# Performance work log

Hardware: AMD Instinct MI355X
Metric: run time of the kernel (lower is better)

The kernel has to match this reference:

```python
import jax, jax.numpy as jnp
import numpy as np

B = 65536
HID = 128
OUT = 10


def setup_inputs() -> dict:
    key = jax.random.key(0)
    ks = jax.random.split(key, 6)
    x = jax.random.normal(ks[0], (B, 784), dtype=jnp.float32)
    conv_w = jax.random.normal(ks[1], (3, 3), dtype=jnp.float32)
    # torch Linear(676,128): weight [128,676], bias [128]
    w1 = jax.random.normal(ks[2], (HID, 26 * 26), dtype=jnp.float32) * (1.0 / np.sqrt(26 * 26))
    b1 = jax.random.normal(ks[3], (HID,), dtype=jnp.float32) * 0.01
    w2 = jax.random.normal(ks[4], (OUT, HID), dtype=jnp.float32) * (1.0 / np.sqrt(HID))
    b2 = jax.random.normal(ks[5], (OUT,), dtype=jnp.float32) * 0.01
    return {"x": x, "conv_w": conv_w, "w1": w1, "b1": b1, "w2": w2, "b2": b2}


def reference(x, conv_w, w1, b1, w2, b2):
    b = x.shape[0]
    img = x.reshape(b, 1, 28, 28)                      # NCHW, single channel
    kern = conv_w.reshape(1, 1, 3, 3)                  # OIHW
    # valid 3x3 cross-correlation (matches the elementwise-multiply-and-sum loop)
    conv = jax.lax.conv_general_dilated(
        img, kern, window_strides=(1, 1), padding="VALID",
        dimension_numbers=("NCHW", "OIHW", "NCHW"))   # [B,1,26,26]
    feat = conv.reshape(b, 26 * 26)
    h = jax.nn.relu(feat @ w1.T + b1)                  # [B,128]
    return h @ w2.T + b2                               # [B,10]
```

## Files before the change

kernel.cpp:

```cpp
#include <hip/hip_runtime.h>
#include <hip/hip_bf16.h>

#define BATCH  65536
#define KREAL  784
#define BK     64
#define NCHUNK 13
#define HID    128
#define NOUT   10
#define BM     128
#define NTHR   512

using f32x4  = __attribute__((ext_vector_type(4))) float;
using short8 = __attribute__((ext_vector_type(8))) short;
using short4v= __attribute__((ext_vector_type(4))) short;
using f4     = __attribute__((ext_vector_type(4))) float;

__device__ inline short f2b(float f) {
    union { __hip_bfloat16 h; short s; } u;
    u.h = __float2bfloat16(f);
    return u.s;
}

#define GLDS16(gp, lp) \
    __builtin_amdgcn_global_load_lds((const __attribute__((address_space(1))) void*)(gp), \
                                     (__attribute__((address_space(3))) void*)(lp), 16, 0, 0)

#define NWB (NCHUNK*HID*BK)
#define NW2 (4*4*16*8)

__global__ void prep_kernel(const float* __restrict__ conv_w,
                            const float* __restrict__ w1,
                            const float* __restrict__ w2,
                            unsigned short* __restrict__ weff_sw,
                            unsigned short* __restrict__ w2f)
{
    int idx = blockIdx.x * 256 + threadIdx.x;
    if (idx < NWB) {
        int ic  = idx >> 13;
        int rem = idx & 8191;
        int r   = rem >> 6;
        int cc  = rem & 63;
        int g   = (cc >> 3) ^ (r & 7);
        int k   = ic * BK + g * 8 + (cc & 7);
        float acc = 0.f;
        if (k < KREAL) {
            int rr = k / 28, c = k - rr * 28;
            #pragma unroll
            for (int di = 0; di < 3; ++di) {
                int i = rr - di;
                if (i >= 0 && i < 26) {
                    #pragma unroll
                    for (int dj = 0; dj < 3; ++dj) {
                        int j = c - dj;
                        if (j >= 0 && j < 26)
                            acc = fmaf(w1[r * 676 + i * 26 + j], conv_w[di * 3 + dj], acc);
                    }
                }
            }
        }
        weff_sw[idx] = (unsigned short)f2b(acc);
    } else {
        int k2 = idx - NWB;
        if (k2 < NW2) {
            int e  = k2 & 7;
            int lo = (k2 >> 3) & 15;
            int hi = (k2 >> 7) & 3;
            int kk = k2 >> 9;
            float v = (lo < NOUT) ? w2[lo * HID + kk * 32 + hi * 8 + e] : 0.f;
            w2f[k2] = (unsigned short)f2b(v);
        }
    }
}

__global__ __launch_bounds__(NTHR, 2)
void fused_mlp_kernel(const float* __restrict__ x,
                      const float* __restrict__ b1,
                      const float* __restrict__ b2,
                      const unsigned short* __restrict__ weff_sw,
                      const unsigned short* __restrict__ w2f,
                      float* __restrict__ out)
{
    extern __shared__ __align__(16) unsigned char smem[];
    unsigned short* ldsA  = (unsigned short*)smem;
    unsigned short* ldsB0 = (unsigned short*)(smem + 65536);
    unsigned short* ldsB1 = (unsigned short*)(smem + 81920);
    unsigned short* ldsH  = (unsigned short*)smem;
    float*          outS  = (float*)(smem + 65536);

    const int tid  = threadIdx.x;
    const int wv   = tid >> 6;
    const int lane = tid & 63;
    const int lo   = lane & 15;
    const int hi   = lane >> 4;
    const int row0 = blockIdx.x * BM;
    const int wr0  = wv * 16;

    f32x4 acc[8];
    #pragma unroll
    for (int t = 0; t < 8; ++t) acc[t] = (f32x4){0.f, 0.f, 0.f, 0.f};

    f4 av[16];
    const char* abase = (const char*)x + (long)(row0 + wr0) * (KREAL * 4);
    auto issueA = [&](int sc) {
        #pragma unroll
        for (int j = 0; j < 16; ++j) {
            int ce = sc * 256 + lane * 4;
            int cb = (ce + 4 <= KREAL) ? ce : 0;
            av[j] = *(const f4*)(abase + (long)j * (KREAL * 4) + (long)cb * 4);
        }
    };
    auto writeA = [&]() {
        #pragma unroll
        for (int j = 0; j < 16; ++j) {
            int r = wr0 + j;
            short4v c;
            c[0] = f2b(av[j][0]); c[1] = f2b(av[j][1]);
            c[2] = f2b(av[j][2]); c[3] = f2b(av[j][3]);
            int byteoff = r * 512 + ((((lane >> 1) ^ (r & 15)) << 4)) + ((lane & 1) << 3);
            *(short4v*)((char*)ldsA + byteoff) = c;
        }
    };
    auto stageB = [&](int ic, unsigned short* dst) {
        const char* src = (const char*)(weff_sw + (long)ic * (HID * BK));
        GLDS16(src + wv * 2048 + lane * 16,        (char*)dst + wv * 2048);
        GLDS16(src + wv * 2048 + 1024 + lane * 16, (char*)dst + wv * 2048 + 1024);
    };

    stageB(0, ldsB0);
    issueA(0);
    asm volatile("s_waitcnt vmcnt(0)" ::: "memory");
    __builtin_amdgcn_sched_barrier(0);
    writeA();
    __builtin_amdgcn_s_barrier();
    __builtin_amdgcn_sched_barrier(0);

    #pragma unroll
    for (int c = 0; c < NCHUNK; ++c) {
        const int sc = c >> 2;
        const int u  = c & 3;
        const unsigned short* Bc = (c & 1) ? ldsB1 : ldsB0;

        if (c + 1 < NCHUNK)
            stageB(c + 1, (c & 1) ? ldsB0 : ldsB1);
        if (u == 2 && sc < 3)
            issueA(sc + 1);

        const int r = wr0 + lo;
        #pragma unroll
        for (int kk = 0; kk < 2; ++kk) {
            const int GA = u * 8 + kk * 4 + hi;
            short8 af = *(const short8*)((const char*)ldsA + r * 512 + ((GA ^ (r & 15)) << 4));
            const int GB = kk * 4 + hi;
            #pragma unroll
            for (int t = 0; t < 8; ++t) {
                const int ob = t * 16 + lo;
                short8 bfrag = *(const short8*)&Bc[ob * BK + ((GB ^ (ob & 7)) << 3)];
                acc[t] = __builtin_amdgcn_mfma_f32_16x16x32_bf16(af, bfrag, acc[t], 0, 0, 0);
            }
        }

        if (c + 1 < NCHUNK) {
            __builtin_amdgcn_sched_barrier(0);
            if (u == 3) {
                asm volatile("s_waitcnt vmcnt(2)" ::: "memory");
                __builtin_amdgcn_sched_barrier(0);
                writeA();
                __builtin_amdgcn_sched_barrier(0);
                asm volatile("s_waitcnt vmcnt(0)" ::: "memory");
            } else if (u == 2) {
                asm volatile("s_waitcnt vmcnt(16)" ::: "memory");
            } else {
                asm volatile("s_waitcnt vmcnt(0)" ::: "memory");
            }
            __builtin_amdgcn_sched_barrier(0);
            __builtin_amdgcn_s_barrier();
            __builtin_amdgcn_sched_barrier(0);
        }
    }

    __builtin_amdgcn_sched_barrier(0);
    __builtin_amdgcn_s_barrier();
    __builtin_amdgcn_sched_barrier(0);

    #pragma unroll
    for (int t = 0; t < 8; ++t) {
        float bias = b1[t * 16 + lo];
        #pragma unroll
        for (int j = 0; j < 4; ++j) {
            float hv = acc[t][j] + bias;
            hv = hv > 0.f ? hv : 0.f;
            int rloc = wr0 + hi * 4 + j;
            int col  = t * 16 + lo;
            int g    = col >> 3, e = col & 7;
            ldsH[rloc * HID + ((g ^ (rloc & 7)) << 3) + e] = (unsigned short)f2b(hv);
        }
    }

    f32x4 acc2 = (f32x4){0.f, 0.f, 0.f, 0.f};
    #pragma unroll
    for (int kk = 0; kk < 4; ++kk) {
        int r = wr0 + lo;
        int g = kk * 4 + hi;
        short8 ha = *(const short8*)&ldsH[r * HID + ((g ^ (r & 7)) << 3)];
        short8 wb = *(const short8*)(w2f + (((kk * 4 + hi) * 16 + lo) << 3));
        acc2 = __builtin_amdgcn_mfma_f32_16x16x32_bf16(ha, wb, acc2, 0, 0, 0);
    }
    float* os = outS + wv * 160;
    if (lo < NOUT) {
        float bb = b2[lo];
        #pragma unroll
        for (int j = 0; j < 4; ++j)
            os[(hi * 4 + j) * NOUT + lo] = acc2[j] + bb;
    }
    if (lane < 40) {
        f4 v = *(const f4*)&os[lane * 4];
        *(f4*)(out + (long)(row0 + wr0) * NOUT + lane * 4) = v;
    }
}

extern "C" void kernel_launch(void* const* d_in, const int* in_sizes, int n_in,
                              void* d_out, int out_size, void* d_ws, size_t ws_size,
                              hipStream_t stream)
{
    const float* x      = (const float*)d_in[0];
    const float* conv_w = (const float*)d_in[1];
    const float* w1     = (const float*)d_in[2];
    const float* b1     = (const float*)d_in[3];
    const float* w2     = (const float*)d_in[4];
    const float* b2     = (const float*)d_in[5];
    float* out = (float*)d_out;

    unsigned short* weff_sw = (unsigned short*)d_ws;
    unsigned short* w2f     = weff_sw + NWB;

    const int prep_total = NWB + NW2;
    prep_kernel<<<(prep_total + 255) / 256, 256, 0, stream>>>(conv_w, w1, w2, weff_sw, w2f);
    fused_mlp_kernel<<<BATCH / BM, NTHR, 98304, stream>>>(x, b1, b2, weff_sw, w2f, out);
}
```

Before: 53.23 us.

## Double block rows to 256 and widen K chunks to 128

Each block now covers 256 rows, with every wave computing two 16-row M tiles that share each B fragment, so B traffic from LDS and global memory per row is halved. The K chunk grows to 128, so there are 7 chunks instead of 13 and fewer barriers. A is loaded per chunk and written to LDS right after the MFMAs. LDS use rises to 128KB, which limits occupancy to one block per CU, and the last chunk only runs its valid K slice. Fewer blocks and less overlap may offset the gain.

```diff
diff --git a/kernel.cpp b/kernel.cpp
--- a/kernel.cpp
+++ b/kernel.cpp
@@ -3,11 +3,11 @@
 
 #define BATCH  65536
 #define KREAL  784
-#define BK     64
-#define NCHUNK 13
+#define BKW    128
+#define NCH    7
 #define HID    128
 #define NOUT   10
-#define BM     128
+#define BM     256
 #define NTHR   512
 
 using f32x4  = __attribute__((ext_vector_type(4))) float;
@@ -25,7 +25,7 @@
     __builtin_amdgcn_global_load_lds((const __attribute__((address_space(1))) void*)(gp), \
                                      (__attribute__((address_space(3))) void*)(lp), 16, 0, 0)
 
-#define NWB (NCHUNK*HID*BK)
+#define NWB (NCH*HID*BKW)
 #define NW2 (4*4*16*8)
 
 __global__ void prep_kernel(const float* __restrict__ conv_w,
@@ -36,12 +36,12 @@
 {
     int idx = blockIdx.x * 256 + threadIdx.x;
     if (idx < NWB) {
-        int ic  = idx >> 13;
-        int rem = idx & 8191;
-        int r   = rem >> 6;
-        int cc  = rem & 63;
-        int g   = (cc >> 3) ^ (r & 7);
-        int k   = ic * BK + g * 8 + (cc & 7);
+        int ic  = idx >> 14;
+        int rem = idx & 16383;
+        int r   = rem >> 7;
+        int cc  = rem & 127;
+        int g   = (cc >> 3) ^ (r & 15);
+        int k   = ic * BKW + g * 8 + (cc & 7);
         float acc = 0.f;
         if (k < KREAL) {
             int rr = k / 28, c = k - rr * 28;
@@ -83,7 +83,7 @@
     extern __shared__ __align__(16) unsigned char smem[];
     unsigned short* ldsA  = (unsigned short*)smem;
     unsigned short* ldsB0 = (unsigned short*)(smem + 65536);
-    unsigned short* ldsB1 = (unsigned short*)(smem + 81920);
+    unsigned short* ldsB1 = (unsigned short*)(smem + 98304);
     unsigned short* ldsH  = (unsigned short*)smem;
     float*          outS  = (float*)(smem + 65536);
 
@@ -93,128 +93,132 @@
     const int lo   = lane & 15;
     const int hi   = lane >> 4;
     const int row0 = blockIdx.x * BM;
-    const int wr0  = wv * 16;
-
-    f32x4 acc[8];
-    #pragma unroll
-    for (int t = 0; t < 8; ++t) acc[t] = (f32x4){0.f, 0.f, 0.f, 0.f};
+    const int wr0  = wv * 32;
+
+    f32x4 acc[2][8];
+    #pragma unroll
+    for (int m = 0; m < 2; ++m)
+        #pragma unroll
+        for (int t = 0; t < 8; ++t) acc[m][t] = (f32x4){0.f, 0.f, 0.f, 0.f};
 
     f4 av[16];
     const char* abase = (const char*)x + (long)(row0 + wr0) * (KREAL * 4);
-    auto issueA = [&](int sc) {
+    auto issueA = [&](int c) {
         #pragma unroll
         for (int j = 0; j < 16; ++j) {
-            int ce = sc * 256 + lane * 4;
+            int rr = j * 2 + (lane >> 5);
+            int ce = c * BKW + (lane & 31) * 4;
             int cb = (ce + 4 <= KREAL) ? ce : 0;
-            av[j] = *(const f4*)(abase + (long)j * (KREAL * 4) + (long)cb * 4);
+            av[j] = *(const f4*)(abase + (long)rr * (KREAL * 4) + (long)cb * 4);
         }
     };
     auto writeA = [&]() {
         #pragma unroll
         for (int j = 0; j < 16; ++j) {
-            int r = wr0 + j;
+            int r  = wr0 + j * 2 + (lane >> 5);
+            int sg = (lane & 31) >> 1;
             short4v c;
             c[0] = f2b(av[j][0]); c[1] = f2b(av[j][1]);
             c[2] = f2b(av[j][2]); c[3] = f2b(av[j][3]);
-            int byteoff = r * 512 + ((((lane >> 1) ^ (r & 15)) << 4)) + ((lane & 1) << 3);
+            int byteoff = r * 256 + ((sg ^ (r & 15)) << 4) + ((lane & 1) << 3);
             *(short4v*)((char*)ldsA + byteoff) = c;
         }
     };
-    auto stageB = [&](int ic, unsigned short* dst) {
-        const char* src = (const char*)(weff_sw + (long)ic * (HID * BK));
-        GLDS16(src + wv * 2048 + lane * 16,        (char*)dst + wv * 2048);
-        GLDS16(src + wv * 2048 + 1024 + lane * 16, (char*)dst + wv * 2048 + 1024);
+    auto stageB = [&](int c, unsigned short* dst) {
+        const char* src = (const char*)(weff_sw + (long)c * (HID * BKW));
+        #pragma unroll
+        for (int q = 0; q < 4; ++q)
+            GLDS16(src + q * 8192 + wv * 1024 + lane * 16,
+                   (char*)dst + q * 8192 + wv * 1024);
     };
 
+    issueA(0);
     stageB(0, ldsB0);
-    issueA(0);
+    writeA();
     asm volatile("s_waitcnt vmcnt(0)" ::: "memory");
     __builtin_amdgcn_sched_barrier(0);
-    writeA();
     __builtin_amdgcn_s_barrier();
     __builtin_amdgcn_sched_barrier(0);
 
     #pragma unroll
-    for (int c = 0; c < NCHUNK; ++c) {
-        const int sc = c >> 2;
-        const int u  = c & 3;
+    for (int c = 0; c < NCH; ++c) {
         const unsigned short* Bc = (c & 1) ? ldsB1 : ldsB0;
-
-        if (c + 1 < NCHUNK)
+        if (c + 1 < NCH) {
+            issueA(c + 1);
             stageB(c + 1, (c & 1) ? ldsB0 : ldsB1);
-        if (u == 2 && sc < 3)
-            issueA(sc + 1);
-
-        const int r = wr0 + lo;
-        #pragma unroll
-        for (int kk = 0; kk < 2; ++kk) {
-            const int GA = u * 8 + kk * 4 + hi;
-            short8 af = *(const short8*)((const char*)ldsA + r * 512 + ((GA ^ (r & 15)) << 4));
-            const int GB = kk * 4 + hi;
+        }
+        const int NS = (c == NCH - 1) ? 1 : 4;
+        #pragma unroll
+        for (int ks = 0; ks < NS; ++ks) {
+            const int G  = ks * 4 + hi;
+            const int r0 = wr0 + lo, r1 = wr0 + 16 + lo;
+            short8 af0 = *(const short8*)((const char*)ldsA + r0 * 256 + ((G ^ (r0 & 15)) << 4));
+            short8 af1 = *(const short8*)((const char*)ldsA + r1 * 256 + ((G ^ (r1 & 15)) << 4));
             #pragma unroll
             for (int t = 0; t < 8; ++t) {
                 const int ob = t * 16 + lo;
-                short8 bfrag = *(const short8*)&Bc[ob * BK + ((GB ^ (ob & 7)) << 3)];
-                acc[t] = __builtin_amdgcn_mfma_f32_16x16x32_bf16(af, bfrag, acc[t], 0, 0, 0);
+                short8 bf = *(const short8*)((const char*)Bc + ob * 256 + ((G ^ (ob & 15)) << 4));
+                acc[0][t] = __builtin_amdgcn_mfma_f32_16x16x32_bf16(af0, bf, acc[0][t], 0, 0, 0);
+                acc[1][t] = __builtin_amdgcn_mfma_f32_16x16x32_bf16(af1, bf, acc[1][t], 0, 0, 0);
             }
         }
-
-        if (c + 1 < NCHUNK) {
-            __builtin_amdgcn_sched_barrier(0);
-            if (u == 3) {
-                asm volatile("s_waitcnt vmcnt(2)" ::: "memory");
-                __builtin_amdgcn_sched_barrier(0);
-                writeA();
-                __builtin_amdgcn_sched_barrier(0);
-                asm volatile("s_waitcnt vmcnt(0)" ::: "memory");
-            } else if (u == 2) {
-                asm volatile("s_waitcnt vmcnt(16)" ::: "memory");
-            } else {
-                asm volatile("s_waitcnt vmcnt(0)" ::: "memory");
+        if (c + 1 < NCH) {
+            __builtin_amdgcn_sched_barrier(0);
+            writeA();
+            __builtin_amdgcn_sched_barrier(0);
+            asm volatile("s_waitcnt vmcnt(0)" ::: "memory");
+            __builtin_amdgcn_sched_barrier(0);
+            __builtin_amdgcn_s_barrier();
+            __builtin_amdgcn_sched_barrier(0);
+        }
+    }
+
+    __builtin_amdgcn_sched_barrier(0);
+    __builtin_amdgcn_s_barrier();
+    __builtin_amdgcn_sched_barrier(0);
+
+    #pragma unroll
+    for (int m = 0; m < 2; ++m) {
+        #pragma unroll
+        for (int t = 0; t < 8; ++t) {
+            float bias = b1[t * 16 + lo];
+            #pragma unroll
+            for (int j = 0; j < 4; ++j) {
+                float hv = acc[m][t][j] + bias;
+                hv = hv > 0.f ? hv : 0.f;
+                int rloc = wr0 + m * 16 + hi * 4 + j;
+                int col  = t * 16 + lo;
+                int g    = col >> 3, e = col & 7;
+                ldsH[rloc * HID + ((g ^ (rloc & 7)) << 3) + e] = (unsigned short)f2b(hv);
             }
-            __builtin_amdgcn_sched_barrier(0);
-            __builtin_amdgcn_s_barrier();
-            __builtin_amdgcn_sched_barrier(0);
-        }
-    }
-
-    __builtin_amdgcn_sched_barrier(0);
-    __builtin_amdgcn_s_barrier();
-    __builtin_amdgcn_sched_barrier(0);
-
-    #pragma unroll
-    for (int t = 0; t < 8; ++t) {
-        float bias = b1[t * 16 + lo];
-        #pragma unroll
-        for (int j = 0; j < 4; ++j) {
-            float hv = acc[t][j] + bias;
-            hv = hv > 0.f ? hv : 0.f;
-            int rloc = wr0 + hi * 4 + j;
-            int col  = t * 16 + lo;
-            int g    = col >> 3, e = col & 7;
-            ldsH[rloc * HID + ((g ^ (rloc & 7)) << 3) + e] = (unsigned short)f2b(hv);
-        }
-    }
-
-    f32x4 acc2 = (f32x4){0.f, 0.f, 0.f, 0.f};
-    #pragma unroll
-    for (int kk = 0; kk < 4; ++kk) {
-        int r = wr0 + lo;
-        int g = kk * 4 + hi;
-        short8 ha = *(const short8*)&ldsH[r * HID + ((g ^ (r & 7)) << 3)];
-        short8 wb = *(const short8*)(w2f + (((kk * 4 + hi) * 16 + lo) << 3));
-        acc2 = __builtin_amdgcn_mfma_f32_16x16x32_bf16(ha, wb, acc2, 0, 0, 0);
-    }
-    float* os = outS + wv * 160;
-    if (lo < NOUT) {
-        float bb = b2[lo];
-        #pragma unroll
-        for (int j = 0; j < 4; ++j)
-            os[(hi * 4 + j) * NOUT + lo] = acc2[j] + bb;
-    }
-    if (lane < 40) {
-        f4 v = *(const f4*)&os[lane * 4];
-        *(f4*)(out + (long)(row0 + wr0) * NOUT + lane * 4) = v;
+        }
+    }
+
+    float* os = outS + wv * 320;
+    #pragma unroll
+    for (int m = 0; m < 2; ++m) {
+        f32x4 acc2 = (f32x4){0.f, 0.f, 0.f, 0.f};
+        #pragma unroll
+        for (int kk = 0; kk < 4; ++kk) {
+            int r = wr0 + m * 16 + lo;
+            int g = kk * 4 + hi;
+            short8 ha = *(const short8*)&ldsH[r * HID + ((g ^ (r & 7)) << 3)];
+            short8 wb = *(const short8*)(w2f + (((kk * 4 + hi) * 16 + lo) << 3));
+            acc2 = __builtin_amdgcn_mfma_f32_16x16x32_bf16(ha, wb, acc2, 0, 0, 0);
+        }
+        if (lo < NOUT) {
+            float bb = b2[lo];
+            #pragma unroll
+            for (int j = 0; j < 4; ++j)
+                os[(m * 16 + hi * 4 + j) * NOUT + lo] = acc2[j] + bb;
+        }
+    }
+    #pragma unroll
+    for (int s = 0; s < 2; ++s) {
+        if (lane < 40) {
+            f4 v = *(const f4*)&os[s * 160 + lane * 4];
+            *(f4*)(out + (long)(row0 + wr0 + s * 16) * NOUT + lane * 4) = v;
+        }
     }
 }
 
@@ -235,5 +239,5 @@
 
     const int prep_total = NWB + NW2;
     prep_kernel<<<(prep_total + 255) / 256, 256, 0, stream>>>(conv_w, w1, w2, weff_sw, w2f);
-    fused_mlp_kernel<<<BATCH / BM, NTHR, 98304, stream>>>(x, b1, b2, weff_sw, w2f, out);
-}
+    fused_mlp_kernel<<<BATCH / BM, NTHR, 131072, stream>>>(x, b1, b2, weff_sw, w2f, out);
+}
```

Result: faster. 49.44 us (-7.1%).
